# Kernel optimization log

Hardware: AMD Instinct MI355X
Metric: run time of the kernel (lower is better)

The kernel has to match this reference:

```python
import jax, jax.numpy as jnp
import numpy as np

# dims: L=tgt len, S=src len, N=batch, E=embed, H=heads
L, S, N, E, H = 1024, 1024, 4, 1024, 16
HD = E // H  # head dim = 64


def setup_inputs() -> dict:
    key = jax.random.key(0)
    ks = jax.random.split(key, 7)
    w_scale = 0.02
    return {
        "query": jax.random.normal(ks[0], (L, N, E), jnp.float32),
        "key": jax.random.normal(ks[1], (S, N, E), jnp.float32),
        "value": jax.random.normal(ks[2], (S, N, E), jnp.float32),
        "in_proj_weight": jax.random.normal(ks[3], (3 * E, E), jnp.float32) * w_scale,
        "in_proj_bias": jax.random.normal(ks[4], (3 * E,), jnp.float32) * w_scale,
        "out_proj_weight": jax.random.normal(ks[5], (E, E), jnp.float32) * w_scale,
        "out_proj_bias": jax.random.normal(ks[6], (E,), jnp.float32) * w_scale,
    }


def reference(query, key, value, in_proj_weight, in_proj_bias,
              out_proj_weight, out_proj_bias):
    scaling = float(HD) ** -0.5
    # packed QKV projection, sliced exactly as the torch code does
    q = (query @ in_proj_weight[:E].T + in_proj_bias[:E]) * scaling        # (L,N,E)
    k = key @ in_proj_weight[E:2 * E].T + in_proj_bias[E:2 * E]            # (S,N,E)
    v = value @ in_proj_weight[2 * E:].T + in_proj_bias[2 * E:]            # (S,N,E)
    # split heads: (L,N,E) -> (N*H, L, HD)
    q = q.reshape(L, N * H, HD).transpose(1, 0, 2)
    k = k.reshape(S, N * H, HD).transpose(1, 0, 2)
    v = v.reshape(S, N * H, HD).transpose(1, 0, 2)
    scores = jnp.einsum('bld,bsd->bls', q, k)          # (N*H, L, S)
    attn = jax.nn.softmax(scores, axis=-1)
    sig = jax.nn.sigmoid(scores)                        # the need_sigmoid_weights variant
    out = jnp.einsum('bls,bsd->bld', attn, v)          # (N*H, L, HD)
    out = out.transpose(1, 0, 2).reshape(L, N, E)
    out = out @ out_proj_weight.T + out_proj_bias       # (L,N,E)
    # weights averaged over heads, as torch MHA returns: (N,L,S)
    attn_weights = attn.reshape(N, H, L, S).sum(axis=1) / H
    sig_weights = sig.reshape(N, H, L, S).sum(axis=1) / H
    return out, attn_weights, sig_weights
```

## Files before the change

kernel.cpp:

```cpp
#include <hip/hip_runtime.h>

#define L_DIM 1024
#define E_DIM 1024
#define NB 4
#define H_NUM 16
#define HD_DIM 64
#define T_TOK 4096
#define NHB 64

typedef float f32x4 __attribute__((ext_vector_type(4)));
typedef unsigned short u16x8 __attribute__((ext_vector_type(8)));
typedef unsigned short u16x4 __attribute__((ext_vector_type(4)));
typedef __bf16 bf16x8 __attribute__((ext_vector_type(8)));

__device__ inline unsigned short f2bf(float f) {
  unsigned int u = __builtin_bit_cast(unsigned int, f);
  u += 0x7FFFu + ((u >> 16) & 1u);
  return (unsigned short)(u >> 16);
}
__device__ inline f32x4 mfma16(u16x8 a, u16x8 b, f32x4 c) {
  return __builtin_amdgcn_mfma_f32_16x16x32_bf16(
      __builtin_bit_cast(bf16x8, a), __builtin_bit_cast(bf16x8, b), c, 0, 0, 0);
}

__device__ __forceinline__ void gl2lds16(const void* g, void* l) {
  auto gp = reinterpret_cast<const __attribute__((address_space(1))) unsigned int*>(
      reinterpret_cast<unsigned long long>(g));
  auto lp = reinterpret_cast<__attribute__((address_space(3))) unsigned int*>(
      static_cast<unsigned int>(reinterpret_cast<unsigned long long>(l)));
  __builtin_amdgcn_global_load_lds(gp, lp, 16, 0, 0);
}

__global__ __launch_bounds__(256) void cast_kernel(
    const float* __restrict__ s0, const float* __restrict__ s1,
    const float* __restrict__ s2, const float* __restrict__ s3,
    unsigned short* __restrict__ d0, unsigned short* __restrict__ d1,
    unsigned short* __restrict__ d2, unsigned short* __restrict__ d3,
    int n0, int n1, int n2, int n3) {
  const int y = blockIdx.y;
  const float* s = (y == 0) ? s0 : (y == 1) ? s1 : (y == 2) ? s2 : s3;
  unsigned short* d = (y == 0) ? d0 : (y == 1) ? d1 : (y == 2) ? d2 : d3;
  const int n = (y == 0) ? n0 : (y == 1) ? n1 : (y == 2) ? n2 : n3;
  int idx = (blockIdx.x * 256 + threadIdx.x) * 8;
  const int stride = gridDim.x * 256 * 8;
  for (; idx < n; idx += stride) {
    float4 a = *(const float4*)(s + idx);
    float4 b = *(const float4*)(s + idx + 4);
    u16x8 o = {f2bf(a.x), f2bf(a.y), f2bf(a.z), f2bf(a.w),
               f2bf(b.x), f2bf(b.y), f2bf(b.z), f2bf(b.w)};
    *(u16x8*)(d + idx) = o;
  }
}

__device__ __forceinline__ void stage_tile(const unsigned short* __restrict__ g,
                                           unsigned short* lbuf, int tid) {
  const int r = tid >> 2, c = tid & 3;
  const int sc = c ^ ((r ^ (r >> 2)) & 3);
  gl2lds16(g + (size_t)r * 1024 + sc * 8, lbuf + tid * 8);
  const int r2 = r + 64;
  gl2lds16(g + (size_t)r2 * 1024 + sc * 8, lbuf + (tid + 256) * 8);
}
__device__ __forceinline__ int frag_off(int r, int q) {
  return r * 32 + ((q ^ ((r ^ (r >> 2)) & 3)) << 3);
}

__global__ __launch_bounds__(256) void qkv_gemm(
    const unsigned short* __restrict__ qb, const unsigned short* __restrict__ kb,
    const unsigned short* __restrict__ vb, const unsigned short* __restrict__ Wb,
    const float* __restrict__ bias, unsigned short* __restrict__ q_hm,
    unsigned short* __restrict__ k_hm, unsigned short* __restrict__ v_t) {
  __shared__ __align__(16) unsigned short As[2][4096];
  __shared__ __align__(16) unsigned short Bs[2][4096];
  const int tid = threadIdx.x;
  const int bm = blockIdx.x, bn = blockIdx.y, z = blockIdx.z;
  const unsigned short* Ag = ((z == 0) ? qb : (z == 1) ? kb : vb) + (size_t)bm * 128 * 1024;
  const unsigned short* Bg = Wb + (size_t)z * 1048576 + (size_t)bn * 128 * 1024;
  const float* bc = bias + z * E_DIM;

  const int w = tid >> 6, lane = tid & 63;
  const int wm = w & 1, wn = w >> 1;
  const int quad = lane >> 4, l16 = lane & 15;

  f32x4 acc[4][4];
#pragma unroll
  for (int i = 0; i < 4; i++)
#pragma unroll
    for (int j = 0; j < 4; j++) { f32x4 zz = {0.f, 0.f, 0.f, 0.f}; acc[i][j] = zz; }

  stage_tile(Ag, As[0], tid);
  stage_tile(Bg, Bs[0], tid);

  for (int kk = 0; kk < 32; kk++) {
    __syncthreads();
    if (kk + 1 < 32) {
      const int bf = (kk + 1) & 1;
      stage_tile(Ag + (kk + 1) * 32, As[bf], tid);
      stage_tile(Bg + (kk + 1) * 32, Bs[bf], tid);
    }
    const int cb = kk & 1;
    u16x8 af[4], bfv[4];
#pragma unroll
    for (int mi = 0; mi < 4; mi++) {
      int r = wm * 64 + mi * 16 + l16;
      af[mi] = *(const u16x8*)&As[cb][frag_off(r, quad)];
    }
#pragma unroll
    for (int ni = 0; ni < 4; ni++) {
      int r = wn * 64 + ni * 16 + l16;
      bfv[ni] = *(const u16x8*)&Bs[cb][frag_off(r, quad)];
    }
#pragma unroll
    for (int mi = 0; mi < 4; mi++)
#pragma unroll
      for (int ni = 0; ni < 4; ni++)
        acc[mi][ni] = mfma16(af[mi], bfv[ni], acc[mi][ni]);
  }
#pragma unroll
  for (int ni = 0; ni < 4; ni++) {
    int col = bn * 128 + wn * 64 + ni * 16 + l16;
    float bv = bc[col];
    int h = col >> 6, d = col & 63;
#pragma unroll
    for (int mi = 0; mi < 4; mi++) {
#pragma unroll
      for (int r = 0; r < 4; r++) {
        int t = bm * 128 + wm * 64 + mi * 16 + quad * 4 + r;
        float v = acc[mi][ni][r] + bv;
        int nb = t & 3, pos = t >> 2;
        if (z == 0) {
          v *= 0.125f;
          q_hm[(size_t)((nb * 16 + h) * 1024 + pos) * 64 + d] = f2bf(v);
        } else if (z == 1) {
          k_hm[(size_t)((nb * 16 + h) * 1024 + pos) * 64 + d] = f2bf(v);
        } else {
          v_t[(size_t)((nb * 16 + h) * 64 + d) * 1024 + pos] = f2bf(v);
        }
      }
    }
  }
}

__global__ __launch_bounds__(256, 3) void attn_kernel(
    const unsigned short* __restrict__ q_hm, const unsigned short* __restrict__ k_hm,
    const unsigned short* __restrict__ v_t, unsigned short* __restrict__ o_h,
    float* __restrict__ m_ws, float* __restrict__ r_ws) {
  __shared__ __align__(16) unsigned short stage[2][4096];
  __shared__ __align__(16) unsigned short sc[16][1032];
  __shared__ float red_m[4][16];
  __shared__ float red_s[4][16];

  const int tid = threadIdx.x;
  const int l0 = blockIdx.x * 16;
  const int b = blockIdx.y;
  const int nb = b >> 4, h = b & 15;
  const int w = tid >> 6, lane = tid & 63;
  const int quad = lane >> 4, l16 = lane & 15;

  const int i1 = tid + 256;
  const int r0s = tid >> 3, c0s = tid & 7;
  const int r1s = i1 >> 3, c1s = i1 & 7;
  const int src0 = (c0s ^ (r0s & 7)) * 8;
  const int src1 = (c1s ^ (r1s & 7)) * 8;

  const unsigned short* kbase = k_hm + ((size_t)b << 16);
  const unsigned short* vbase = v_t + ((size_t)b << 16);

  const unsigned short* qp = q_hm + ((size_t)(b * 1024 + l0 + l16) << 6) + quad * 8;
  u16x8 bq0 = *(const u16x8*)qp;
  u16x8 bq1 = *(const u16x8*)(qp + 32);

  f32x4 acc[16];
#pragma unroll
  for (int j = 0; j < 16; j++) { f32x4 z = {0.f, 0.f, 0.f, 0.f}; acc[j] = z; }

  gl2lds16(kbase + ((size_t)r0s << 6) + src0, &stage[0][tid * 8]);
  gl2lds16(kbase + ((size_t)r1s << 6) + src1, &stage[0][i1 * 8]);

  const int myrow = w * 16 + l16;
  const int sw0 = ((quad ^ (l16 & 7)) * 8);
  const int sw1 = (((quad + 4) ^ (l16 & 7)) * 8);

#pragma unroll
  for (int j = 0; j < 16; j++) {
    __syncthreads();
    if (j + 1 < 16) {
      int bf = (j + 1) & 1;
      gl2lds16(kbase + ((size_t)((j + 1) * 64 + r0s) << 6) + src0, &stage[bf][tid * 8]);
      gl2lds16(kbase + ((size_t)((j + 1) * 64 + r1s) << 6) + src1, &stage[bf][i1 * 8]);
    }
    const unsigned short* kt = &stage[j & 1][myrow * 64];
    u16x8 ak0 = *(const u16x8*)(kt + sw0);
    u16x8 ak1 = *(const u16x8*)(kt + sw1);
    acc[j] = mfma16(ak0, bq0, acc[j]);
    acc[j] = mfma16(ak1, bq1, acc[j]);
  }

  gl2lds16(vbase + ((size_t)r0s << 10) + src0, &stage[0][tid * 8]);
  gl2lds16(vbase + ((size_t)r1s << 10) + src1, &stage[0][i1 * 8]);

  float lm = -1e30f;
#pragma unroll
  for (int j = 0; j < 16; j++)
    for (int r = 0; r < 4; r++) lm = fmaxf(lm, acc[j][r]);
  lm = fmaxf(lm, __shfl_xor(lm, 16, 64));
  lm = fmaxf(lm, __shfl_xor(lm, 32, 64));
  if (lane < 16) red_m[w][lane] = lm;
  __syncthreads();
  float m4 = fmaxf(fmaxf(red_m[0][l16], red_m[1][l16]),
                   fmaxf(red_m[2][l16], red_m[3][l16]));

  float ls = 0.f;
#pragma unroll
  for (int j = 0; j < 16; j++) {
    float e0 = __expf(acc[j][0] - m4);
    float e1 = __expf(acc[j][1] - m4);
    float e2 = __expf(acc[j][2] - m4);
    float e3 = __expf(acc[j][3] - m4);
    ls += (e0 + e1) + (e2 + e3);
    u16x4 p = {f2bf(e0), f2bf(e1), f2bf(e2), f2bf(e3)};
    *(u16x4*)&sc[l16][j * 64 + w * 16 + quad * 4] = p;
  }
  ls += __shfl_xor(ls, 16, 64);
  ls += __shfl_xor(ls, 32, 64);
  if (lane < 16) red_s[w][lane] = ls;
  __syncthreads();
  float s4 = red_s[0][l16] + red_s[1][l16] + red_s[2][l16] + red_s[3][l16];
  float rv = 1.0f / s4;
  if (w == 0 && lane < 16) {
    m_ws[b * 1024 + l0 + lane] = m4;
    r_ws[b * 1024 + l0 + lane] = rv;
  }

  f32x4 oacc = {0.f, 0.f, 0.f, 0.f};
  const unsigned short* scrow = &sc[l16][0];
#pragma unroll
  for (int j = 0; j < 16; j++) {
    __syncthreads();
    if (j + 1 < 16) {
      int bf = (j + 1) & 1;
      gl2lds16(vbase + ((size_t)r0s << 10) + (j + 1) * 64 + src0, &stage[bf][tid * 8]);
      gl2lds16(vbase + ((size_t)r1s << 10) + (j + 1) * 64 + src1, &stage[bf][i1 * 8]);
    }
    const unsigned short* vt = &stage[j & 1][myrow * 64];
    u16x8 bv0 = *(const u16x8*)(vt + sw0);
    u16x8 bv1 = *(const u16x8*)(vt + sw1);
    u16x8 ap0 = *(const u16x8*)(scrow + j * 64 + quad * 8);
    u16x8 ap1 = *(const u16x8*)(scrow + j * 64 + 32 + quad * 8);
    oacc = mfma16(ap0, bv0, oacc);
    oacc = mfma16(ap1, bv1, oacc);
  }

#pragma unroll
  for (int r = 0; r < 4; r++) {
    int lr = quad * 4 + r;
    float rvr = __shfl(rv, lr, 64);
    float val = oacc[r] * rvr;
    int t = (l0 + lr) * 4 + nb;
    o_h[((size_t)t << 10) + h * 64 + w * 16 + l16] = f2bf(val);
  }
}

__global__ __launch_bounds__(256) void weights_kernel(
    const unsigned short* __restrict__ q_hm, const unsigned short* __restrict__ k_hm,
    const float* __restrict__ m_ws, const float* __restrict__ r_ws,
    float* __restrict__ attn_out, float* __restrict__ sig_out) {
  __shared__ __align__(16) unsigned short qs[2][4096];
  __shared__ __align__(16) unsigned short ks[2][4096];
  __shared__ float ml[16][64];
  __shared__ float rl[16][64];
  __shared__ float cl[16][64];

  const int tid = threadIdx.x;
  const int s0 = blockIdx.x * 64;
  const int l0 = blockIdx.y * 64;
  const int nb = blockIdx.z;
  const int w = tid >> 6, lane = tid & 63;
  const int quad = lane >> 4, l16 = lane & 15;

  const int i1 = tid + 256;
  const int r0s = tid >> 3, c0s = tid & 7;
  const int r1s = i1 >> 3, c1s = i1 & 7;
  const int src0 = (c0s ^ (r0s & 7)) * 8;
  const int src1 = (c1s ^ (r1s & 7)) * 8;

  {
    int idx = tid * 4;
    int hh = idx >> 6, ii = idx & 63;
    int bb = nb * 16 + hh;
    float4 mv4 = *(const float4*)&m_ws[bb * 1024 + l0 + ii];
    float4 rv4 = *(const float4*)&r_ws[bb * 1024 + l0 + ii];
    *(float4*)&ml[hh][ii] = mv4;
    *(float4*)&rl[hh][ii] = rv4;
    float4 cv4 = {__expf(-mv4.x), __expf(-mv4.y), __expf(-mv4.z), __expf(-mv4.w)};
    *(float4*)&cl[hh][ii] = cv4;
  }

  {
    int bb = nb * 16;
    const unsigned short* qb = q_hm + ((size_t)(bb * 1024 + l0) << 6);
    const unsigned short* kb = k_hm + ((size_t)(bb * 1024 + s0) << 6);
    gl2lds16(qb + (r0s << 6) + src0, &qs[0][tid * 8]);
    gl2lds16(qb + (r1s << 6) + src1, &qs[0][i1 * 8]);
    gl2lds16(kb + (r0s << 6) + src0, &ks[0][tid * 8]);
    gl2lds16(kb + (r1s << 6) + src1, &ks[0][i1 * 8]);
  }

  const int sw0 = ((quad ^ (l16 & 7)) * 8);
  const int sw1 = (((quad + 4) ^ (l16 & 7)) * 8);

  f32x4 accA[4], accS[4];
#pragma unroll
  for (int i = 0; i < 4; i++) {
    f32x4 zz = {0.f, 0.f, 0.f, 0.f};
    accA[i] = zz; accS[i] = zz;
  }

#pragma unroll
  for (int h = 0; h < 16; h++) {
    __syncthreads();
    if (h + 1 < 16) {
      int bf = (h + 1) & 1;
      int bb = nb * 16 + h + 1;
      const unsigned short* qb = q_hm + ((size_t)(bb * 1024 + l0) << 6);
      const unsigned short* kb = k_hm + ((size_t)(bb * 1024 + s0) << 6);
      gl2lds16(qb + (r0s << 6) + src0, &qs[bf][tid * 8]);
      gl2lds16(qb + (r1s << 6) + src1, &qs[bf][i1 * 8]);
      gl2lds16(kb + (r0s << 6) + src0, &ks[bf][tid * 8]);
      gl2lds16(kb + (r1s << 6) + src1, &ks[bf][i1 * 8]);
    }
    const int bf = h & 1;
    const unsigned short* qt = &qs[bf][(w * 16 + l16) * 64];
    u16x8 a0 = *(const u16x8*)(qt + sw0);
    u16x8 a1 = *(const u16x8*)(qt + sw1);
    f32x4 mv = *(const f32x4*)&ml[h][w * 16 + quad * 4];
    f32x4 rv = *(const f32x4*)&rl[h][w * 16 + quad * 4];
    f32x4 cv = *(const f32x4*)&cl[h][w * 16 + quad * 4];
#pragma unroll
    for (int ni = 0; ni < 4; ni++) {
      const unsigned short* kt = &ks[bf][(ni * 16 + l16) * 64];
      u16x8 b0 = *(const u16x8*)(kt + sw0);
      u16x8 b1 = *(const u16x8*)(kt + sw1);
      f32x4 scv = {0.f, 0.f, 0.f, 0.f};
      scv = mfma16(a0, b0, scv);
      scv = mfma16(a1, b1, scv);
#pragma unroll
      for (int r = 0; r < 4; r++) {
        float e = __expf(scv[r] - mv[r]);
        accA[ni][r] += e * rv[r];
        accS[ni][r] += e * __builtin_amdgcn_rcpf(e + cv[r]);
      }
    }
  }
  const float inv_h = 1.0f / 16.0f;
  const int lrow0 = l0 + w * 16;
#pragma unroll
  for (int ni = 0; ni < 4; ni++) {
#pragma unroll
    for (int r = 0; r < 4; r++) {
      int l = lrow0 + quad * 4 + r;
      int s = s0 + ni * 16 + l16;
      size_t idx = ((size_t)nb * 1024 + l) * 1024 + s;
      attn_out[idx] = accA[ni][r] * inv_h;
      sig_out[idx] = accS[ni][r] * inv_h;
    }
  }
}

__global__ __launch_bounds__(256) void out_gemm(
    const unsigned short* __restrict__ o_h, const unsigned short* __restrict__ Wb,
    const float* __restrict__ bias, float* __restrict__ out) {
  __shared__ __align__(16) unsigned short As[2][4096];
  __shared__ __align__(16) unsigned short Bs[2][4096];
  const int tid = threadIdx.x;
  const int bm = blockIdx.x, bn = blockIdx.y;
  const unsigned short* Ag = o_h + (size_t)bm * 128 * 1024;
  const unsigned short* Bg = Wb + (size_t)bn * 128 * 1024;

  const int w = tid >> 6, lane = tid & 63;
  const int wm = w & 1, wn = w >> 1;
  const int quad = lane >> 4, l16 = lane & 15;

  f32x4 acc[4][4];
#pragma unroll
  for (int i = 0; i < 4; i++)
#pragma unroll
    for (int j = 0; j < 4; j++) { f32x4 zz = {0.f, 0.f, 0.f, 0.f}; acc[i][j] = zz; }

  stage_tile(Ag, As[0], tid);
  stage_tile(Bg, Bs[0], tid);

  for (int kk = 0; kk < 32; kk++) {
    __syncthreads();
    if (kk + 1 < 32) {
      const int bf = (kk + 1) & 1;
      stage_tile(Ag + (kk + 1) * 32, As[bf], tid);
      stage_tile(Bg + (kk + 1) * 32, Bs[bf], tid);
    }
    const int cb = kk & 1;
    u16x8 af[4], bfv[4];
#pragma unroll
    for (int mi = 0; mi < 4; mi++) {
      int r = wm * 64 + mi * 16 + l16;
      af[mi] = *(const u16x8*)&As[cb][frag_off(r, quad)];
    }
#pragma unroll
    for (int ni = 0; ni < 4; ni++) {
      int r = wn * 64 + ni * 16 + l16;
      bfv[ni] = *(const u16x8*)&Bs[cb][frag_off(r, quad)];
    }
#pragma unroll
    for (int mi = 0; mi < 4; mi++)
#pragma unroll
      for (int ni = 0; ni < 4; ni++)
        acc[mi][ni] = mfma16(af[mi], bfv[ni], acc[mi][ni]);
  }
#pragma unroll
  for (int ni = 0; ni < 4; ni++) {
    int col = bn * 128 + wn * 64 + ni * 16 + l16;
    float bv = bias[col];
#pragma unroll
    for (int mi = 0; mi < 4; mi++) {
#pragma unroll
      for (int r = 0; r < 4; r++) {
        int t = bm * 128 + wm * 64 + mi * 16 + quad * 4 + r;
        out[(size_t)t * E_DIM + col] = acc[mi][ni][r] + bv;
      }
    }
  }
}

extern "C" void kernel_launch(void* const* d_in, const int* in_sizes, int n_in,
                              void* d_out, int out_size, void* d_ws, size_t ws_size,
                              hipStream_t stream) {
  const float* qin  = (const float*)d_in[0];
  const float* kin  = (const float*)d_in[1];
  const float* vin  = (const float*)d_in[2];
  const float* Wqkv = (const float*)d_in[3];
  const float* bqkv = (const float*)d_in[4];
  const float* Wout = (const float*)d_in[5];
  const float* bout = (const float*)d_in[6];
  float* out      = (float*)d_out;
  float* attn_out = out + 4194304;
  float* sig_out  = out + 8388608;

  unsigned short* q_hm = (unsigned short*)d_ws;
  unsigned short* k_hm = q_hm + 4194304;
  unsigned short* v_t  = q_hm + 8388608;
  unsigned short* o_h  = q_hm + 12582912;
  float* m_ws = (float*)(q_hm + 16777216);
  float* r_ws = m_ws + 65536;

  unsigned short* qb = (unsigned short*)(out + 4194304);
  unsigned short* kb = qb + 4194304;
  unsigned short* vb = qb + 8388608;
  unsigned short* Wqkvb = o_h;
  unsigned short* Woutb = v_t;

  cast_kernel<<<dim3(2048, 4), 256, 0, stream>>>(
      qin, kin, vin, Wqkv, qb, kb, vb, Wqkvb,
      4194304, 4194304, 4194304, 3145728);
  qkv_gemm<<<dim3(32, 8, 3), 256, 0, stream>>>(qb, kb, vb, Wqkvb, bqkv,
                                               q_hm, k_hm, v_t);
  attn_kernel<<<dim3(64, 64), 256, 0, stream>>>(q_hm, k_hm, v_t, o_h, m_ws, r_ws);
  cast_kernel<<<dim3(512, 1), 256, 0, stream>>>(
      Wout, Wout, Wout, Wout, Woutb, Woutb, Woutb, Woutb,
      1048576, 0, 0, 0);
  weights_kernel<<<dim3(16, 16, 4), 256, 0, stream>>>(q_hm, k_hm, m_ws, r_ws,
                                                      attn_out, sig_out);
  out_gemm<<<dim3(32, 8), 256, 0, stream>>>(o_h, Woutb, bout, out);
}
```

Measured before the change: 306.6 us.

## Process 32 query rows per attention block and keep probabilities in registers

Each attention block now handles 32 query rows instead of 16, so each K/V tile staged in LDS feeds twice as many MFMAs and total K/V global traffic is halved. The full-row bf16 probability buffer in shared memory is replaced by a small double-buffered per-tile buffer filled from register-held exponentials during the PV loop. The first V tile load is also moved into the last QK iteration. The cost is doubled accumulator registers, occupancy dropped to 2 blocks per SM, and half as many blocks in the grid.

After: 291.1 us. 1.05x faster.

```diff
diff --git a/kernel.cpp b/kernel.cpp
--- a/kernel.cpp
+++ b/kernel.cpp
@@ -140,17 +140,17 @@
   }
 }
 
-__global__ __launch_bounds__(256, 3) void attn_kernel(
+__global__ __launch_bounds__(256, 2) void attn_kernel(
     const unsigned short* __restrict__ q_hm, const unsigned short* __restrict__ k_hm,
     const unsigned short* __restrict__ v_t, unsigned short* __restrict__ o_h,
     float* __restrict__ m_ws, float* __restrict__ r_ws) {
   __shared__ __align__(16) unsigned short stage[2][4096];
-  __shared__ __align__(16) unsigned short sc[16][1032];
-  __shared__ float red_m[4][16];
-  __shared__ float red_s[4][16];
+  __shared__ __align__(16) unsigned short pt[2][32][68];
+  __shared__ float red_m[4][32];
+  __shared__ float red_s[4][32];
 
   const int tid = threadIdx.x;
-  const int l0 = blockIdx.x * 16;
+  const int l0 = blockIdx.x * 32;
   const int b = blockIdx.y;
   const int nb = b >> 4, h = b & 15;
   const int w = tid >> 6, lane = tid & 63;
@@ -165,13 +165,20 @@
   const unsigned short* kbase = k_hm + ((size_t)b << 16);
   const unsigned short* vbase = v_t + ((size_t)b << 16);
 
-  const unsigned short* qp = q_hm + ((size_t)(b * 1024 + l0 + l16) << 6) + quad * 8;
-  u16x8 bq0 = *(const u16x8*)qp;
-  u16x8 bq1 = *(const u16x8*)(qp + 32);
-
-  f32x4 acc[16];
-#pragma unroll
-  for (int j = 0; j < 16; j++) { f32x4 z = {0.f, 0.f, 0.f, 0.f}; acc[j] = z; }
+  u16x8 bq[2][2];
+#pragma unroll
+  for (int g = 0; g < 2; g++) {
+    const unsigned short* qp =
+        q_hm + ((size_t)(b * 1024 + l0 + g * 16 + l16) << 6) + quad * 8;
+    bq[g][0] = *(const u16x8*)qp;
+    bq[g][1] = *(const u16x8*)(qp + 32);
+  }
+
+  f32x4 acc[16][2];
+#pragma unroll
+  for (int j = 0; j < 16; j++)
+#pragma unroll
+    for (int g = 0; g < 2; g++) { f32x4 z = {0.f, 0.f, 0.f, 0.f}; acc[j][g] = z; }
 
   gl2lds16(kbase + ((size_t)r0s << 6) + src0, &stage[0][tid * 8]);
   gl2lds16(kbase + ((size_t)r1s << 6) + src1, &stage[0][i1 * 8]);
@@ -183,80 +190,117 @@
 #pragma unroll
   for (int j = 0; j < 16; j++) {
     __syncthreads();
-    if (j + 1 < 16) {
+    if (j < 15) {
       int bf = (j + 1) & 1;
       gl2lds16(kbase + ((size_t)((j + 1) * 64 + r0s) << 6) + src0, &stage[bf][tid * 8]);
       gl2lds16(kbase + ((size_t)((j + 1) * 64 + r1s) << 6) + src1, &stage[bf][i1 * 8]);
+    } else {
+      gl2lds16(vbase + ((size_t)r0s << 10) + src0, &stage[0][tid * 8]);
+      gl2lds16(vbase + ((size_t)r1s << 10) + src1, &stage[0][i1 * 8]);
     }
     const unsigned short* kt = &stage[j & 1][myrow * 64];
     u16x8 ak0 = *(const u16x8*)(kt + sw0);
     u16x8 ak1 = *(const u16x8*)(kt + sw1);
-    acc[j] = mfma16(ak0, bq0, acc[j]);
-    acc[j] = mfma16(ak1, bq1, acc[j]);
-  }
-
-  gl2lds16(vbase + ((size_t)r0s << 10) + src0, &stage[0][tid * 8]);
-  gl2lds16(vbase + ((size_t)r1s << 10) + src1, &stage[0][i1 * 8]);
-
-  float lm = -1e30f;
+    acc[j][0] = mfma16(ak0, bq[0][0], acc[j][0]);
+    acc[j][0] = mfma16(ak1, bq[0][1], acc[j][0]);
+    acc[j][1] = mfma16(ak0, bq[1][0], acc[j][1]);
+    acc[j][1] = mfma16(ak1, bq[1][1], acc[j][1]);
+  }
+
+  float lm0 = -3e38f, lm1 = -3e38f;
 #pragma unroll
   for (int j = 0; j < 16; j++)
-    for (int r = 0; r < 4; r++) lm = fmaxf(lm, acc[j][r]);
-  lm = fmaxf(lm, __shfl_xor(lm, 16, 64));
-  lm = fmaxf(lm, __shfl_xor(lm, 32, 64));
-  if (lane < 16) red_m[w][lane] = lm;
+#pragma unroll
+    for (int r = 0; r < 4; r++) {
+      lm0 = fmaxf(lm0, acc[j][0][r]);
+      lm1 = fmaxf(lm1, acc[j][1][r]);
+    }
+  lm0 = fmaxf(lm0, __shfl_xor(lm0, 16, 64));
+  lm0 = fmaxf(lm0, __shfl_xor(lm0, 32, 64));
+  lm1 = fmaxf(lm1, __shfl_xor(lm1, 16, 64));
+  lm1 = fmaxf(lm1, __shfl_xor(lm1, 32, 64));
+  if (lane < 16) { red_m[w][lane] = lm0; red_m[w][lane + 16] = lm1; }
   __syncthreads();
-  float m4 = fmaxf(fmaxf(red_m[0][l16], red_m[1][l16]),
+  float m0 = fmaxf(fmaxf(red_m[0][l16], red_m[1][l16]),
                    fmaxf(red_m[2][l16], red_m[3][l16]));
-
-  float ls = 0.f;
+  float m1 = fmaxf(fmaxf(red_m[0][l16 + 16], red_m[1][l16 + 16]),
+                   fmaxf(red_m[2][l16 + 16], red_m[3][l16 + 16]));
+
+  float ls0 = 0.f, ls1 = 0.f;
 #pragma unroll
   for (int j = 0; j < 16; j++) {
-    float e0 = __expf(acc[j][0] - m4);
-    float e1 = __expf(acc[j][1] - m4);
-    float e2 = __expf(acc[j][2] - m4);
-    float e3 = __expf(acc[j][3] - m4);
-    ls += (e0 + e1) + (e2 + e3);
-    u16x4 p = {f2bf(e0), f2bf(e1), f2bf(e2), f2bf(e3)};
-    *(u16x4*)&sc[l16][j * 64 + w * 16 + quad * 4] = p;
-  }
-  ls += __shfl_xor(ls, 16, 64);
-  ls += __shfl_xor(ls, 32, 64);
-  if (lane < 16) red_s[w][lane] = ls;
+#pragma unroll
+    for (int r = 0; r < 4; r++) {
+      float e0 = __expf(acc[j][0][r] - m0);
+      float e1 = __expf(acc[j][1][r] - m1);
+      acc[j][0][r] = e0;
+      acc[j][1][r] = e1;
+      ls0 += e0;
+      ls1 += e1;
+    }
+  }
+  ls0 += __shfl_xor(ls0, 16, 64);
+  ls0 += __shfl_xor(ls0, 32, 64);
+  ls1 += __shfl_xor(ls1, 16, 64);
+  ls1 += __shfl_xor(ls1, 32, 64);
+  if (lane < 16) { red_s[w][lane] = ls0; red_s[w][lane + 16] = ls1; }
   __syncthreads();
-  float s4 = red_s[0][l16] + red_s[1][l16] + red_s[2][l16] + red_s[3][l16];
-  float rv = 1.0f / s4;
-  if (w == 0 && lane < 16) {
-    m_ws[b * 1024 + l0 + lane] = m4;
-    r_ws[b * 1024 + l0 + lane] = rv;
-  }
-
-  f32x4 oacc = {0.f, 0.f, 0.f, 0.f};
-  const unsigned short* scrow = &sc[l16][0];
+  float rv0 = 1.0f / (red_s[0][l16] + red_s[1][l16] + red_s[2][l16] + red_s[3][l16]);
+  float rv1 = 1.0f / (red_s[0][l16 + 16] + red_s[1][l16 + 16] +
+                      red_s[2][l16 + 16] + red_s[3][l16 + 16]);
+  if (tid < 32) {
+    float mm = fmaxf(fmaxf(red_m[0][tid], red_m[1][tid]),
+                     fmaxf(red_m[2][tid], red_m[3][tid]));
+    float ss = red_s[0][tid] + red_s[1][tid] + red_s[2][tid] + red_s[3][tid];
+    m_ws[b * 1024 + l0 + tid] = mm;
+    r_ws[b * 1024 + l0 + tid] = 1.0f / ss;
+  }
+
+  {
+    u16x4 p0 = {f2bf(acc[0][0][0]), f2bf(acc[0][0][1]), f2bf(acc[0][0][2]), f2bf(acc[0][0][3])};
+    u16x4 p1 = {f2bf(acc[0][1][0]), f2bf(acc[0][1][1]), f2bf(acc[0][1][2]), f2bf(acc[0][1][3])};
+    *(u16x4*)&pt[0][l16][w * 16 + quad * 4] = p0;
+    *(u16x4*)&pt[0][16 + l16][w * 16 + quad * 4] = p1;
+  }
+
+  f32x4 oacc0 = {0.f, 0.f, 0.f, 0.f};
+  f32x4 oacc1 = {0.f, 0.f, 0.f, 0.f};
 #pragma unroll
   for (int j = 0; j < 16; j++) {
     __syncthreads();
-    if (j + 1 < 16) {
+    if (j < 15) {
       int bf = (j + 1) & 1;
       gl2lds16(vbase + ((size_t)r0s << 10) + (j + 1) * 64 + src0, &stage[bf][tid * 8]);
       gl2lds16(vbase + ((size_t)r1s << 10) + (j + 1) * 64 + src1, &stage[bf][i1 * 8]);
+      u16x4 p0 = {f2bf(acc[j + 1][0][0]), f2bf(acc[j + 1][0][1]),
+                  f2bf(acc[j + 1][0][2]), f2bf(acc[j + 1][0][3])};
+      u16x4 p1 = {f2bf(acc[j + 1][1][0]), f2bf(acc[j + 1][1][1]),
+                  f2bf(acc[j + 1][1][2]), f2bf(acc[j + 1][1][3])};
+      *(u16x4*)&pt[bf][l16][w * 16 + quad * 4] = p0;
+      *(u16x4*)&pt[bf][16 + l16][w * 16 + quad * 4] = p1;
     }
     const unsigned short* vt = &stage[j & 1][myrow * 64];
     u16x8 bv0 = *(const u16x8*)(vt + sw0);
     u16x8 bv1 = *(const u16x8*)(vt + sw1);
-    u16x8 ap0 = *(const u16x8*)(scrow + j * 64 + quad * 8);
-    u16x8 ap1 = *(const u16x8*)(scrow + j * 64 + 32 + quad * 8);
-    oacc = mfma16(ap0, bv0, oacc);
-    oacc = mfma16(ap1, bv1, oacc);
+    u16x8 ap00 = *(const u16x8*)&pt[j & 1][l16][quad * 8];
+    u16x8 ap01 = *(const u16x8*)&pt[j & 1][l16][32 + quad * 8];
+    u16x8 ap10 = *(const u16x8*)&pt[j & 1][16 + l16][quad * 8];
+    u16x8 ap11 = *(const u16x8*)&pt[j & 1][16 + l16][32 + quad * 8];
+    oacc0 = mfma16(ap00, bv0, oacc0);
+    oacc0 = mfma16(ap01, bv1, oacc0);
+    oacc1 = mfma16(ap10, bv0, oacc1);
+    oacc1 = mfma16(ap11, bv1, oacc1);
   }
 
 #pragma unroll
   for (int r = 0; r < 4; r++) {
     int lr = quad * 4 + r;
-    float rvr = __shfl(rv, lr, 64);
-    float val = oacc[r] * rvr;
-    int t = (l0 + lr) * 4 + nb;
-    o_h[((size_t)t << 10) + h * 64 + w * 16 + l16] = f2bf(val);
+    float rr0 = __shfl(rv0, lr, 64);
+    float rr1 = __shfl(rv1, lr, 64);
+    int t0 = (l0 + lr) * 4 + nb;
+    int t1 = (l0 + 16 + lr) * 4 + nb;
+    o_h[((size_t)t0 << 10) + h * 64 + w * 16 + l16] = f2bf(oacc0[r] * rr0);
+    o_h[((size_t)t1 << 10) + h * 64 + w * 16 + l16] = f2bf(oacc1[r] * rr1);
   }
 }
 
@@ -461,7 +505,7 @@
       4194304, 4194304, 4194304, 3145728);
   qkv_gemm<<<dim3(32, 8, 3), 256, 0, stream>>>(qb, kb, vb, Wqkvb, bqkv,
                                                q_hm, k_hm, v_t);
-  attn_kernel<<<dim3(64, 64), 256, 0, stream>>>(q_hm, k_hm, v_t, o_h, m_ws, r_ws);
+  attn_kernel<<<dim3(32, 64), 256, 0, stream>>>(q_hm, k_hm, v_t, o_h, m_ws, r_ws);
   cast_kernel<<<dim3(512, 1), 256, 0, stream>>>(
       Wout, Wout, Wout, Wout, Woutb, Woutb, Woutb, Woutb,
       1048576, 0, 0, 0);
```
